# Performance work log

Hardware: AMD Instinct MI355X
Metric: run time of the kernel (lower is better)

The kernel has to match this reference:

```python
import jax, jax.numpy as jnp
import numpy as np

D = 256
HEADS = 8
LEVELS = 4
POINTS = 4
HD = D // HEADS  # 32
SHAPES = [(96, 96), (48, 48), (24, 24), (12, 12)]
N_BATCH = 2


def setup_inputs() -> dict:
    key = jax.random.key(0)
    ks = jax.random.split(key, 10)
    Lin = sum(h * w for h, w in SHAPES)  # 12240
    src = jax.random.normal(ks[0], (N_BATCH, Lin, D), jnp.float32)
    reference_points = jax.random.uniform(ks[1], (N_BATCH, Lin, LEVELS, 2), jnp.float32)
    spatial_shapes = np.array(SHAPES, dtype=np.int64)
    level_start_index = np.concatenate([[0], np.cumsum([h * w for h, w in SHAPES])[:-1]]).astype(np.int64)
    s = 0.02
    w_value = s * jax.random.normal(ks[2], (D, D), jnp.float32)
    b_value = jnp.zeros((D,), jnp.float32)
    w_off = s * jax.random.normal(ks[3], (D, HEADS * LEVELS * POINTS * 2), jnp.float32)
    b_off = 0.5 * jax.random.normal(ks[4], (HEADS * LEVELS * POINTS * 2,), jnp.float32)
    w_attn = s * jax.random.normal(ks[5], (D, HEADS * LEVELS * POINTS), jnp.float32)
    b_attn = jnp.zeros((HEADS * LEVELS * POINTS,), jnp.float32)
    w_out = s * jax.random.normal(ks[6], (D, D), jnp.float32)
    b_out = jnp.zeros((D,), jnp.float32)
    gamma = jnp.ones((D,), jnp.float32)
    beta = jnp.zeros((D,), jnp.float32)
    return dict(src=src, reference_points=reference_points, spatial_shapes=spatial_shapes,
                level_start_index=level_start_index, w_value=w_value, b_value=b_value,
                w_off=w_off, b_off=b_off, w_attn=w_attn, b_attn=b_attn,
                w_out=w_out, b_out=b_out, gamma=gamma, beta=beta)


def _bilinear_sample(value_flat, H, W, loc):
    # value_flat: (N, heads, H*W, hd); loc: (N, heads, Lq, P, 2) normalized [0,1]
    # Equivalent to F.grid_sample(bilinear, padding_mode='zeros', align_corners=False)
    x = loc[..., 0] * W - 0.5
    y = loc[..., 1] * H - 0.5
    x0 = jnp.floor(x)
    y0 = jnp.floor(y)
    lx = x - x0
    ly = y - y0
    n, h, Lq, P = x.shape
    out = jnp.zeros((n, h, Lq, P, value_flat.shape[-1]), value_flat.dtype)
    for dy, wy in ((0, 1.0 - ly), (1, ly)):
        for dx, wx in ((0, 1.0 - lx), (1, lx)):
            xi = x0 + dx
            yi = y0 + dy
            valid = (xi >= 0) & (xi < W) & (yi >= 0) & (yi < H)
            idx = (jnp.clip(yi, 0, H - 1) * W + jnp.clip(xi, 0, W - 1)).astype(jnp.int32)
            v = jnp.take_along_axis(value_flat, idx.reshape(n, h, Lq * P, 1), axis=2)
            v = v.reshape(n, h, Lq, P, -1)
            out = out + v * (wx * wy * valid.astype(value_flat.dtype))[..., None]
    return out


def reference(src, reference_points, spatial_shapes, level_start_index,
              w_value, b_value, w_off, b_off, w_attn, b_attn, w_out, b_out, gamma, beta):
    N, Lq, _ = src.shape
    shapes = np.asarray(spatial_shapes)
    starts = np.asarray(level_start_index)

    # projections
    value = (src @ w_value + b_value).reshape(N, Lq, HEADS, HD)
    offsets = (src @ w_off + b_off).reshape(N, Lq, HEADS, LEVELS, POINTS, 2)
    attn = (src @ w_attn + b_attn).reshape(N, Lq, HEADS, LEVELS * POINTS)
    attn = jax.nn.softmax(attn, axis=-1).reshape(N, Lq, HEADS, LEVELS, POINTS)

    # sampling locations: ref + offset / (W_l, H_l)
    normalizer = jnp.asarray(shapes[:, ::-1].copy(), jnp.float32)  # (L, 2) = (W, H)
    loc = reference_points[:, :, None, :, None, :] + offsets / normalizer[None, None, None, :, None, :]

    out = jnp.zeros((N, HEADS, Lq, HD), src.dtype)
    for l in range(LEVELS):
        H, W = int(shapes[l, 0]), int(shapes[l, 1])
        s0 = int(starts[l])
        v_l = value[:, s0:s0 + H * W].transpose(0, 2, 1, 3)        # (N, heads, HW, hd)
        loc_l = loc[:, :, :, l].transpose(0, 2, 1, 3, 4)           # (N, heads, Lq, P, 2)
        sampled = _bilinear_sample(v_l, H, W, loc_l)               # (N, heads, Lq, P, hd)
        w_l = attn[:, :, :, l].transpose(0, 2, 1, 3)               # (N, heads, Lq, P)
        out = out + (sampled * w_l[..., None]).sum(axis=3)
    out = out.transpose(0, 2, 1, 3).reshape(N, Lq, D)
    out = out @ w_out + b_out

    # residual (dropout in eval = identity) + LayerNorm
    x = src + out
    mu = x.mean(-1, keepdims=True)
    var = x.var(-1, keepdims=True)
    return (x - mu) / jnp.sqrt(var + 1e-5) * gamma + beta
```

## Files before the change

kernel.cpp:

```cpp
#include <hip/hip_runtime.h>
#include <cstdint>
#include <cstddef>

#define D 256
#define HEADS 8
#define HD 32
#define NB 2
#define LQ 12240
#define NQ (NB * LQ)
#define PLANE (LQ * HD)

typedef __attribute__((ext_vector_type(8))) short bf16x8;
typedef __attribute__((ext_vector_type(4))) float f32x4;
typedef __bf16 bf16x2 __attribute__((ext_vector_type(2)));

__device__ __forceinline__ ushort f2bf(float f) {
    union { float f; uint32_t u; } c; c.f = f;
    uint32_t u = c.u;
    uint32_t r = (u + 0x7fffu + ((u >> 16) & 1u)) >> 16;
    return (ushort)r;
}
__device__ __forceinline__ float bflo(uint32_t u) { return __uint_as_float(u << 16); }
__device__ __forceinline__ float bfhi(uint32_t u) { return __uint_as_float(u & 0xffff0000u); }

__device__ __forceinline__ float dot2bf(uint32_t a, uint32_t b, float c) {
#if __has_builtin(__builtin_amdgcn_fdot2_f32_bf16)
    return __builtin_amdgcn_fdot2_f32_bf16(__builtin_bit_cast(bf16x2, a),
                                           __builtin_bit_cast(bf16x2, b), c, false);
#else
    return c + bflo(a) * bflo(b) + bfhi(a) * bfhi(b);
#endif
}

__global__ __launch_bounds__(256) void conv_kernel(
    const float* __restrict__ w_value, const float* __restrict__ w_off,
    const float* __restrict__ w_attn,  const float* __restrict__ b_value,
    const float* __restrict__ b_off,   const float* __restrict__ b_attn,
    const float* __restrict__ w_out,   const float* __restrict__ src,
    ushort* __restrict__ B_pack, ushort* __restrict__ w_out_t,
    float* __restrict__ b_pack, ushort* __restrict__ src_bf)
{
    const int b = blockIdx.x, k = threadIdx.x;
    if (b >= 899) {
        const size_t i = ((size_t)(b - 899) * 256 + k) * 4;
        float4 v = *(const float4*)(src + i);
        ushort4 o;
        o.x = f2bf(v.x); o.y = f2bf(v.y); o.z = f2bf(v.z); o.w = f2bf(v.w);
        *(ushort4*)(src_bf + i) = o;
        return;
    }
    if (b < 640) {
        float v;
        if (b < 256)      v = w_value[(size_t)k * 256 + b];
        else if (b < 512) v = w_off[(size_t)k * 256 + (b - 256)];
        else              v = w_attn[(size_t)k * 128 + (b - 512)];
        B_pack[(size_t)b * 256 + k] = f2bf(v);
    } else if (b < 896) {
        int n = b - 640;
        w_out_t[(size_t)n * 256 + k] = f2bf(w_out[(size_t)k * 256 + n]);
    } else if (b == 896) {
        b_pack[k] = b_value[k];
    } else if (b == 897) {
        b_pack[256 + k] = b_off[k];
    } else {
        if (k < 128) b_pack[512 + k] = b_attn[k];
    }
}

__global__ __launch_bounds__(256, 2) void proj_gemm(
    const ushort* __restrict__ src_bf, const ushort* __restrict__ B_pack,
    const float* __restrict__ b_pack,
    ushort* __restrict__ val_t, float* __restrict__ off_raw,
    float* __restrict__ attn_raw)
{
    const int tid = threadIdx.x;
    const int wv = tid >> 6, lane = tid & 63;
    const int quad = lane >> 4, ln = lane & 15;
    const int mc = blockIdx.x;
    const int by = blockIdx.y;

    const ushort* bp = B_pack + (size_t)(by * 64 + ln) * 256 + quad * 8;
    bf16x8 bfr[4][8];
#pragma unroll
    for (int t = 0; t < 4; ++t)
#pragma unroll
        for (int s = 0; s < 8; ++s)
            bfr[t][s] = *(const bf16x8*)(bp + (size_t)t * (16 * 256) + s * 32);

    float bias[4];
#pragma unroll
    for (int t = 0; t < 4; ++t) bias[t] = b_pack[by * 64 + t * 16 + ln];

    for (int i = 0; i < 6; ++i) {
        const int base = (mc * 6 + i) * 64;
        if (base >= NQ) break;
        const int row_a = base + wv * 16 + ln;
        const bool va = row_a < NQ;
        const ushort* ap = src_bf + (size_t)row_a * 256 + quad * 8;

        bf16x8 af[8];
#pragma unroll
        for (int s = 0; s < 8; ++s) {
            bf16x8 v = {0, 0, 0, 0, 0, 0, 0, 0};
            if (va) v = *(const bf16x8*)(ap + s * 32);
            af[s] = v;
        }

        f32x4 acc[4] = {{0,0,0,0},{0,0,0,0},{0,0,0,0},{0,0,0,0}};
#pragma unroll
        for (int s = 0; s < 8; ++s)
#pragma unroll
            for (int t = 0; t < 4; ++t)
                acc[t] = __builtin_amdgcn_mfma_f32_16x16x32_bf16(af[s], bfr[t][s], acc[t], 0, 0, 0);

        if (by < 4) {
#pragma unroll
            for (int t = 0; t < 4; ++t) {
                const int n_g = by * 64 + t * 16 + ln;
                const int h = n_g >> 5, hd = n_g & 31;
#pragma unroll
                for (int reg = 0; reg < 4; ++reg) {
                    int row = base + wv * 16 + quad * 4 + reg;
                    if (row < NQ) {
                        int nb = row >= LQ; int ql = row - nb * LQ;
                        val_t[(((size_t)(nb * 8 + h)) * LQ + ql) * 32 + hd] =
                            f2bf(acc[t][reg] + bias[t]);
                    }
                }
            }
        } else if (by < 8) {
#pragma unroll
            for (int t = 0; t < 4; ++t) {
                const int col = (by - 4) * 64 + t * 16 + ln;
#pragma unroll
                for (int reg = 0; reg < 4; ++reg) {
                    int row = base + wv * 16 + quad * 4 + reg;
                    if (row < NQ)
                        off_raw[(size_t)row * 256 + col] = acc[t][reg] + bias[t];
                }
            }
        } else {
#pragma unroll
            for (int t = 0; t < 4; ++t) {
                const int col = (by - 8) * 64 + t * 16 + ln;
#pragma unroll
                for (int reg = 0; reg < 4; ++reg) {
                    int row = base + wv * 16 + quad * 4 + reg;
                    if (row < NQ)
                        attn_raw[(size_t)row * 128 + col] = acc[t][reg] + bias[t];
                }
            }
        }
    }
}

__global__ __launch_bounds__(256) void pair_kernel(
    const ushort* __restrict__ val_t, uint32_t* __restrict__ val_pair)
{
    const uint32_t i = blockIdx.x * 256 + threadIdx.x;
    const uint32_t c = i & 31;
    const uint32_t rest = i >> 5;
    const uint32_t plane = rest / LQ;
    const uint32_t pos = rest - plane * LQ;
    int l = (pos >= 9216) + (pos >= 11520) + (pos >= 12096);
    uint32_t s0 = (l > 0 ? 9216u : 0u) + (l > 1 ? 2304u : 0u) + (l > 2 ? 576u : 0u);
    uint32_t Wi = 96u >> l;
    uint32_t p = pos - s0;
    uint32_t q = (p / 3u) >> (5 - l);
    uint32_t xr = p - q * Wi;
    uint32_t nxt = (xr == Wi - 1u) ? pos : pos + 1u;
    uint32_t lo = val_t[(size_t)plane * PLANE + pos * 32 + c];
    uint32_t hi = val_t[(size_t)plane * PLANE + nxt * 32 + c];
    val_pair[i] = lo | (hi << 16);
}

__global__ __launch_bounds__(256) void sample_kernel(
    const float* __restrict__ ref_pts,
    const uint32_t* __restrict__ val_pair,
    const float* __restrict__ off_raw,
    const float* attn_raw,
    uint32_t* sampled)
{
    __shared__ uint32_t sm_i[16][2][18];
    __shared__ uint32_t sm_w[16][2][18];
    const int gl = threadIdx.x >> 4;
    const int ln = threadIdx.x & 15;
    const int h     = blockIdx.x & 7;
    const int chunk = blockIdx.x >> 3;
    const int qg = chunk * 16 + gl;
    const int n  = (qg >= LQ) ? 1 : 0;
    const int l  = ln >> 2;

    float a = attn_raw[(size_t)qg * 128 + h * 16 + ln];
    float m = a;
#pragma unroll
    for (int s = 8; s; s >>= 1) m = fmaxf(m, __shfl_xor(m, s, 16));
    float e = __expf(a - m);
    float ssum = e;
#pragma unroll
    for (int s = 8; s; s >>= 1) ssum += __shfl_xor(ssum, s, 16);
    float aw = e / ssum;

    float ox = off_raw[(size_t)qg * 256 + h * 32 + ln * 2 + 0];
    float oy = off_raw[(size_t)qg * 256 + h * 32 + ln * 2 + 1];
    float rx = ref_pts[(qg * 4 + l) * 2 + 0];
    float ry = ref_pts[(qg * 4 + l) * 2 + 1];

    const int Wi = 96 >> l;
    const int Hi = Wi;
    const int s0 = (l > 0 ? 9216 : 0) + (l > 1 ? 2304 : 0) + (l > 2 ? 576 : 0);
    const float Wf = (float)Wi, Hf = (float)Hi;

    float x = (rx + ox / Wf) * Wf - 0.5f;
    float y = (ry + oy / Hf) * Hf - 0.5f;
    float x0f = floorf(x), y0f = floorf(y);
    float lx = x - x0f, ly = y - y0f;
    int x0 = (int)x0f, y0 = (int)y0f;

    float wy0 = (y0 >= 0 && y0 < Hi) ? (1.f - ly) : 0.f;
    float wy1 = (y0 + 1 >= 0 && y0 + 1 < Hi) ? ly : 0.f;
    int yc0 = min(max(y0, 0), Hi - 1);
    int yc1 = min(max(y0 + 1, 0), Hi - 1);
    float wl = (x0 >= 0 && x0 < Wi) ? (1.f - lx) : 0.f;
    float wh = (x0 + 1 >= 0 && x0 + 1 < Wi) ? lx : 0.f;
    float pl, ph;
    int xe;
    if (x0 < 0) { pl = wh; ph = 0.f; xe = x0 + 1; }
    else        { pl = wl; ph = wh;  xe = x0; }
    int xc = min(max(xe, 0), Wi - 1);
    pl *= aw; ph *= aw;

    sm_i[gl][0][ln] = (uint32_t)(s0 + yc0 * Wi + xc) * 32u;
    sm_i[gl][1][ln] = (uint32_t)(s0 + yc1 * Wi + xc) * 32u;
    sm_w[gl][0][ln] = ((uint32_t)f2bf(ph * wy0) << 16) | (uint32_t)f2bf(pl * wy0);
    sm_w[gl][1][ln] = ((uint32_t)f2bf(ph * wy1) << 16) | (uint32_t)f2bf(pl * wy1);

    const int half = ln >> 3;
    const int cb   = (ln & 7) * 4;
    const uint32_t* plane =
        val_pair + (size_t)(n * HEADS + h) * PLANE + cb;

    float a0 = 0.f, a1 = 0.f, a2 = 0.f, a3 = 0.f;
#pragma unroll
    for (int c = 0; c < 2; ++c) {
        uint4    rv[8];
        uint32_t wpk[8];
#pragma unroll
        for (int p = 0; p < 8; ++p) {
            uint32_t off = sm_i[gl][half][c * 8 + p];
            rv[p]  = *(const uint4*)(plane + off);
            wpk[p] = sm_w[gl][half][c * 8 + p];
        }
#pragma unroll
        for (int p = 0; p < 8; ++p) {
            a0 = dot2bf(rv[p].x, wpk[p], a0);
            a1 = dot2bf(rv[p].y, wpk[p], a1);
            a2 = dot2bf(rv[p].z, wpk[p], a2);
            a3 = dot2bf(rv[p].w, wpk[p], a3);
        }
    }
    a0 += __shfl_xor(a0, 8, 16);
    a1 += __shfl_xor(a1, 8, 16);
    a2 += __shfl_xor(a2, 8, 16);
    a3 += __shfl_xor(a3, 8, 16);
    if (ln < 8) {
        uint2 rr;
        rr.x = ((uint32_t)f2bf(a1) << 16) | (uint32_t)f2bf(a0);
        rr.y = ((uint32_t)f2bf(a3) << 16) | (uint32_t)f2bf(a2);
        *(uint2*)(sampled + (size_t)qg * 128 + h * 16 + 2 * ln) = rr;
    }
}

__global__ __launch_bounds__(256, 2) void out_gemm(
    const ushort* __restrict__ sampled, const ushort* __restrict__ w_out_t,
    const float* __restrict__ b_out,    const float* __restrict__ src,
    float* __restrict__ x)
{
    const int tid = threadIdx.x;
    const int wv = tid >> 6, lane = tid & 63;
    const int quad = lane >> 4, ln = lane & 15;
    const int mc = blockIdx.x;
    const int by = blockIdx.y;

    const ushort* bp = w_out_t + (size_t)(by * 64 + ln) * 256 + quad * 8;
    bf16x8 bfr[4][8];
#pragma unroll
    for (int t = 0; t < 4; ++t)
#pragma unroll
        for (int s = 0; s < 8; ++s)
            bfr[t][s] = *(const bf16x8*)(bp + (size_t)t * (16 * 256) + s * 32);

    float bias[4];
#pragma unroll
    for (int t = 0; t < 4; ++t) bias[t] = b_out[by * 64 + t * 16 + ln];

    for (int i = 0; i < 3; ++i) {
        const int base = (mc * 3 + i) * 64;
        if (base >= NQ) break;
        const int row_a = base + wv * 16 + ln;
        const bool va = row_a < NQ;
        const ushort* ap = sampled + (size_t)row_a * 256 + quad * 8;

        bf16x8 af[8];
#pragma unroll
        for (int s = 0; s < 8; ++s) {
            bf16x8 v = {0, 0, 0, 0, 0, 0, 0, 0};
            if (va) v = *(const bf16x8*)(ap + s * 32);
            af[s] = v;
        }

        f32x4 acc[4] = {{0,0,0,0},{0,0,0,0},{0,0,0,0},{0,0,0,0}};
#pragma unroll
        for (int s = 0; s < 8; ++s)
#pragma unroll
            for (int t = 0; t < 4; ++t)
                acc[t] = __builtin_amdgcn_mfma_f32_16x16x32_bf16(af[s], bfr[t][s], acc[t], 0, 0, 0);

#pragma unroll
        for (int t = 0; t < 4; ++t) {
            const int col = by * 64 + t * 16 + ln;
#pragma unroll
            for (int reg = 0; reg < 4; ++reg) {
                int row = base + wv * 16 + quad * 4 + reg;
                if (row < NQ)
                    x[(size_t)row * 256 + col] =
                        acc[t][reg] + bias[t] + src[(size_t)row * 256 + col];
            }
        }
    }
}

__global__ __launch_bounds__(256) void ln_kernel(
    const float* __restrict__ x, const float* __restrict__ gamma,
    const float* __restrict__ beta, float* __restrict__ out)
{
    const int row  = blockIdx.x * 4 + (threadIdx.x >> 6);
    const int lane = threadIdx.x & 63;
    float4 v = *(const float4*)(x + (size_t)row * 256 + lane * 4);
    float s  = v.x + v.y + v.z + v.w;
    float s2 = v.x * v.x + v.y * v.y + v.z * v.z + v.w * v.w;
#pragma unroll
    for (int o = 32; o; o >>= 1) {
        s  += __shfl_xor(s, o);
        s2 += __shfl_xor(s2, o);
    }
    float mu  = s * (1.f / 256.f);
    float var = s2 * (1.f / 256.f) - mu * mu;
    float rs  = rsqrtf(var + 1e-5f);
    float4 g = *(const float4*)(gamma + lane * 4);
    float4 b = *(const float4*)(beta + lane * 4);
    float4 o4;
    o4.x = (v.x - mu) * rs * g.x + b.x;
    o4.y = (v.y - mu) * rs * g.y + b.y;
    o4.z = (v.z - mu) * rs * g.z + b.z;
    o4.w = (v.w - mu) * rs * g.w + b.w;
    *(float4*)(out + (size_t)row * 256 + lane * 4) = o4;
}

extern "C" void kernel_launch(void* const* d_in, const int* in_sizes, int n_in,
                              void* d_out, int out_size, void* d_ws, size_t ws_size,
                              hipStream_t stream)
{
    const float* src     = (const float*)d_in[0];
    const float* refp    = (const float*)d_in[1];
    const float* w_value = (const float*)d_in[4];
    const float* b_value = (const float*)d_in[5];
    const float* w_off   = (const float*)d_in[6];
    const float* b_off   = (const float*)d_in[7];
    const float* w_attn  = (const float*)d_in[8];
    const float* b_attn  = (const float*)d_in[9];
    const float* w_out   = (const float*)d_in[10];
    const float* b_out   = (const float*)d_in[11];
    const float* gamma   = (const float*)d_in[12];
    const float* beta    = (const float*)d_in[13];

    char* ws = (char*)d_ws;
    ushort*   val_t    = (ushort*)  (ws);
    uint32_t* val_pair = (uint32_t*)(ws + 12533760);
    ushort*   src_bf   = (ushort*)  (ws + 12533760);
    float*    off_raw  = (float*)   (ws + 37601280);
    float*    attn_raw = (float*)   (ws + 62668800);
    uint32_t* sampled  = (uint32_t*)(ws + 62668800);
    ushort*   B_pack   = (ushort*)  (ws + 75202560);
    ushort*   w_out_t  = (ushort*)  (ws + 75530240);
    float*    b_pack   = (float*)   (ws + 75661312);
    float*    x        = off_raw;
    float*    out      = (float*)d_out;

    conv_kernel<<<7019, 256, 0, stream>>>(w_value, w_off, w_attn, b_value, b_off,
                                          b_attn, w_out, src, B_pack, w_out_t,
                                          b_pack, src_bf);
    proj_gemm<<<dim3(64, 10), 256, 0, stream>>>(src_bf, B_pack, b_pack, val_t,
                                                off_raw, attn_raw);
    pair_kernel<<<24480, 256, 0, stream>>>(val_t, val_pair);
    sample_kernel<<<12240, 256, 0, stream>>>(refp, val_pair, off_raw, attn_raw,
                                             sampled);
    out_gemm<<<dim3(128, 4), 256, 0, stream>>>((const ushort*)sampled, w_out_t,
                                               b_out, src, x);
    ln_kernel<<<6120, 256, 0, stream>>>(x, gamma, beta, out);
}
```

Before: 215.0 us.

## Fuse output projection GEMM with residual add and LayerNorm

The output GEMM is restructured so each block computes a full 256-column row tile (64 rows). This lets the residual add and LayerNorm run in registers, using shuffle reductions across 16 lanes, so the separate ln_kernel launch and the fp32 intermediate buffer round-trip go away. In exchange the grid drops from 512 blocks to 383. Weights are now streamed from global memory per k-step rather than kept in registers, and the wider accumulators raise register pressure.

```diff
diff --git a/kernel.cpp b/kernel.cpp
--- a/kernel.cpp
+++ b/kernel.cpp
@@ -271,90 +271,80 @@
     }
 }
 
-__global__ __launch_bounds__(256, 2) void out_gemm(
+__global__ __launch_bounds__(256, 2) void out_ln_gemm(
     const ushort* __restrict__ sampled, const ushort* __restrict__ w_out_t,
     const float* __restrict__ b_out,    const float* __restrict__ src,
-    float* __restrict__ x)
-{
+    const float* __restrict__ gamma,    const float* __restrict__ beta,
+    float* __restrict__ out)
+{
+    __shared__ float sm_gb[3][256];
     const int tid = threadIdx.x;
+    sm_gb[0][tid] = gamma[tid];
+    sm_gb[1][tid] = beta[tid];
+    sm_gb[2][tid] = b_out[tid];
+    __syncthreads();
+
     const int wv = tid >> 6, lane = tid & 63;
     const int quad = lane >> 4, ln = lane & 15;
-    const int mc = blockIdx.x;
-    const int by = blockIdx.y;
-
-    const ushort* bp = w_out_t + (size_t)(by * 64 + ln) * 256 + quad * 8;
-    bf16x8 bfr[4][8];
-#pragma unroll
-    for (int t = 0; t < 4; ++t)
-#pragma unroll
-        for (int s = 0; s < 8; ++s)
-            bfr[t][s] = *(const bf16x8*)(bp + (size_t)t * (16 * 256) + s * 32);
-
-    float bias[4];
-#pragma unroll
-    for (int t = 0; t < 4; ++t) bias[t] = b_out[by * 64 + t * 16 + ln];
-
-    for (int i = 0; i < 3; ++i) {
-        const int base = (mc * 3 + i) * 64;
-        if (base >= NQ) break;
-        const int row_a = base + wv * 16 + ln;
-        const bool va = row_a < NQ;
-        const ushort* ap = sampled + (size_t)row_a * 256 + quad * 8;
-
-        bf16x8 af[8];
-#pragma unroll
-        for (int s = 0; s < 8; ++s) {
+    const int base = blockIdx.x * 64;
+    const int row_a = base + wv * 16 + ln;
+    const bool va = row_a < NQ;
+    const ushort* ap = sampled + (size_t)row_a * 256 + quad * 8;
+
+    f32x4 acc[16];
+#pragma unroll
+    for (int t = 0; t < 16; ++t) acc[t] = (f32x4){0.f, 0.f, 0.f, 0.f};
+
+#pragma unroll
+    for (int sh = 0; sh < 2; ++sh) {
+        bf16x8 af[4];
+#pragma unroll
+        for (int s = 0; s < 4; ++s) {
             bf16x8 v = {0, 0, 0, 0, 0, 0, 0, 0};
-            if (va) v = *(const bf16x8*)(ap + s * 32);
+            if (va) v = *(const bf16x8*)(ap + (sh * 4 + s) * 32);
             af[s] = v;
         }
-
-        f32x4 acc[4] = {{0,0,0,0},{0,0,0,0},{0,0,0,0},{0,0,0,0}};
-#pragma unroll
-        for (int s = 0; s < 8; ++s)
-#pragma unroll
-            for (int t = 0; t < 4; ++t)
-                acc[t] = __builtin_amdgcn_mfma_f32_16x16x32_bf16(af[s], bfr[t][s], acc[t], 0, 0, 0);
-
-#pragma unroll
-        for (int t = 0; t < 4; ++t) {
-            const int col = by * 64 + t * 16 + ln;
-#pragma unroll
-            for (int reg = 0; reg < 4; ++reg) {
-                int row = base + wv * 16 + quad * 4 + reg;
-                if (row < NQ)
-                    x[(size_t)row * 256 + col] =
-                        acc[t][reg] + bias[t] + src[(size_t)row * 256 + col];
-            }
-        }
-    }
-}
-
-__global__ __launch_bounds__(256) void ln_kernel(
-    const float* __restrict__ x, const float* __restrict__ gamma,
-    const float* __restrict__ beta, float* __restrict__ out)
-{
-    const int row  = blockIdx.x * 4 + (threadIdx.x >> 6);
-    const int lane = threadIdx.x & 63;
-    float4 v = *(const float4*)(x + (size_t)row * 256 + lane * 4);
-    float s  = v.x + v.y + v.z + v.w;
-    float s2 = v.x * v.x + v.y * v.y + v.z * v.z + v.w * v.w;
-#pragma unroll
-    for (int o = 32; o; o >>= 1) {
-        s  += __shfl_xor(s, o);
-        s2 += __shfl_xor(s2, o);
-    }
-    float mu  = s * (1.f / 256.f);
-    float var = s2 * (1.f / 256.f) - mu * mu;
-    float rs  = rsqrtf(var + 1e-5f);
-    float4 g = *(const float4*)(gamma + lane * 4);
-    float4 b = *(const float4*)(beta + lane * 4);
-    float4 o4;
-    o4.x = (v.x - mu) * rs * g.x + b.x;
-    o4.y = (v.y - mu) * rs * g.y + b.y;
-    o4.z = (v.z - mu) * rs * g.z + b.z;
-    o4.w = (v.w - mu) * rs * g.w + b.w;
-    *(float4*)(out + (size_t)row * 256 + lane * 4) = o4;
+#pragma unroll
+        for (int s = 0; s < 4; ++s) {
+            const ushort* bp = w_out_t + (size_t)ln * 256 + quad * 8 + (sh * 4 + s) * 32;
+#pragma unroll
+            for (int t = 0; t < 16; ++t) {
+                bf16x8 bf = *(const bf16x8*)(bp + (size_t)t * (16 * 256));
+                acc[t] = __builtin_amdgcn_mfma_f32_16x16x32_bf16(af[s], bf, acc[t], 0, 0, 0);
+            }
+        }
+    }
+
+#pragma unroll
+    for (int reg = 0; reg < 4; ++reg) {
+        const int row = base + wv * 16 + quad * 4 + reg;
+        const bool vr = row < NQ;
+        float s1 = 0.f, s2 = 0.f;
+        if (vr) {
+            const float* sp = src + (size_t)row * 256 + ln;
+#pragma unroll
+            for (int t = 0; t < 16; ++t) {
+                float v = acc[t][reg] + sm_gb[2][t * 16 + ln] + sp[t * 16];
+                acc[t][reg] = v;
+                s1 += v; s2 += v * v;
+            }
+        }
+#pragma unroll
+        for (int o = 8; o; o >>= 1) {
+            s1 += __shfl_xor(s1, o, 16);
+            s2 += __shfl_xor(s2, o, 16);
+        }
+        float mu  = s1 * (1.f / 256.f);
+        float var = s2 * (1.f / 256.f) - mu * mu;
+        float rs  = rsqrtf(var + 1e-5f);
+        if (vr) {
+            float* op = out + (size_t)row * 256 + ln;
+#pragma unroll
+            for (int t = 0; t < 16; ++t)
+                op[t * 16] = (acc[t][reg] - mu) * rs * sm_gb[0][t * 16 + ln]
+                           + sm_gb[1][t * 16 + ln];
+        }
+    }
 }
 
 extern "C" void kernel_launch(void* const* d_in, const int* in_sizes, int n_in,
@@ -384,7 +374,6 @@
     ushort*   B_pack   = (ushort*)  (ws + 75202560);
     ushort*   w_out_t  = (ushort*)  (ws + 75530240);
     float*    b_pack   = (float*)   (ws + 75661312);
-    float*    x        = off_raw;
     float*    out      = (float*)d_out;
 
     conv_kernel<<<7019, 256, 0, stream>>>(w_value, w_off, w_attn, b_value, b_off,
@@ -395,7 +384,6 @@
     pair_kernel<<<24480, 256, 0, stream>>>(val_t, val_pair);
     sample_kernel<<<12240, 256, 0, stream>>>(refp, val_pair, off_raw, attn_raw,
                                              sampled);
-    out_gemm<<<dim3(128, 4), 256, 0, stream>>>((const ushort*)sampled, w_out_t,
-                                               b_out, src, x);
-    ln_kernel<<<6120, 256, 0, stream>>>(x, gamma, beta, out);
-}
+    out_ln_gemm<<<383, 256, 0, stream>>>((const ushort*)sampled, w_out_t,
+                                         b_out, src, gamma, beta, out);
+}
```

Measured after the change: 215.1 us. Within noise of the previous version (+0.0%).
